# Optimization experiments

Measured on AMD Instinct MI355X. Metric: run time of the kernel, lower is better.

Reference implementation:

```python
import jax, jax.numpy as jnp
import numpy as np
import math

EPS = 1.0
DELT = 1e-05
CLIP = 1.0
N_LOCS = 1000000
EMB_DIM = 64
N_EDGES = 4000000


def setup_inputs() -> dict:
    key = jax.random.key(0)
    k1, k2, k3 = jax.random.split(key, 3)
    loc_emb = jax.random.normal(k1, (N_LOCS, EMB_DIM), dtype=jnp.float32)
    noise = jax.random.normal(k2, (N_EDGES, EMB_DIM), dtype=jnp.float32)
    edge_locs = jax.random.randint(k3, (N_EDGES,), 0, N_LOCS, dtype=jnp.int32)
    return {"loc_emb": loc_emb, "noise": noise, "edge_locs": edge_locs}


def reference(loc_emb, noise, edge_locs):
    n_locs = loc_emb.shape[0]
    # sigma = clip * sqrt(2 * ln(1.25/delta)) / eps  (Gaussian mechanism)
    sigma = CLIP * math.sqrt(2.0 * math.log(1.25 / DELT)) / EPS
    # edge_cnt[loc] = number of edges touching loc (Counter over real+fake)
    edge_cnt = jax.ops.segment_sum(
        jnp.ones_like(edge_locs, dtype=loc_emb.dtype), edge_locs,
        num_segments=n_locs)
    # per-edge scaled noise: sigma * n / edge_cnt[loc]; every referenced loc has cnt>=1
    inv_cnt = (sigma / edge_cnt[edge_locs])[:, None]  # [E, 1]
    loc_noise = jax.ops.segment_sum(noise * inv_cnt, edge_locs,
                                    num_segments=n_locs)  # [n_locs, d]
    return loc_emb + loc_noise
```

## Files before the change

kernel.cpp:

```cpp
#include <hip/hip_runtime.h>
#include <math.h>

#define EMB 64

typedef float f32x4 __attribute__((ext_vector_type(4)));


__global__ void count_rank_k(const int* __restrict__ el, int* __restrict__ cnt,
                             int* __restrict__ rank, int n) {
    int i = blockIdx.x * blockDim.x + threadIdx.x;
    if (i < n) rank[i] = atomicAdd(cnt + el[i], 1);
}

__global__ void block_sum_k(const int* __restrict__ cnt, int* __restrict__ part, int n) {
    __shared__ int s[256];
    int i = blockIdx.x * 256 + threadIdx.x;
    s[threadIdx.x] = (i < n) ? cnt[i] : 0;
    __syncthreads();
    for (int off = 128; off > 0; off >>= 1) {
        if (threadIdx.x < off) s[threadIdx.x] += s[threadIdx.x + off];
        __syncthreads();
    }
    if (threadIdx.x == 0) part[blockIdx.x] = s[0];
}

__global__ void scan_part_k(int* __restrict__ part, int nb) {
    __shared__ int s[4096];
    for (int i = threadIdx.x; i < 4096; i += 1024) s[i] = (i < nb) ? part[i] : 0;
    __syncthreads();
    for (int off = 1; off < 4096; off <<= 1) {
        int vals[4];
        #pragma unroll
        for (int j = 0; j < 4; ++j) {
            int i = threadIdx.x + j * 1024;
            vals[j] = (i >= off) ? s[i - off] : 0;
        }
        __syncthreads();
        #pragma unroll
        for (int j = 0; j < 4; ++j) {
            int i = threadIdx.x + j * 1024;
            s[i] += vals[j];
        }
        __syncthreads();
    }
    for (int i = threadIdx.x; i < nb; i += 1024) part[i] = (i == 0) ? 0 : s[i - 1];
}

__global__ void scan_block_k(const int* __restrict__ cnt, const int* __restrict__ part,
                             int* __restrict__ offs, int n) {
    __shared__ int s[256];
    int i = blockIdx.x * 256 + threadIdx.x;
    int v = (i < n) ? cnt[i] : 0;
    s[threadIdx.x] = v;
    __syncthreads();
    for (int off = 1; off < 256; off <<= 1) {
        int t = (threadIdx.x >= (unsigned)off) ? s[threadIdx.x - off] : 0;
        __syncthreads();
        s[threadIdx.x] += t;
        __syncthreads();
    }
    if (i < n) offs[i] = s[threadIdx.x] - v + part[blockIdx.x];
}

__global__ void fill_csr_k(const int* __restrict__ el, const int* __restrict__ rank,
                           const int* __restrict__ offs, int* __restrict__ csr, int n) {
    int i = blockIdx.x * blockDim.x + threadIdx.x;
    if (i < n) csr[offs[el[i]] + rank[i]] = i;
}


__device__ __forceinline__ f32x4 ld_row(const float* noise, int e, int q) {
    return *(reinterpret_cast<const f32x4*>(noise + ((long long)e << 6)) + q);
}

__global__ void gather_k(const float* __restrict__ loc_emb, const float* __restrict__ noise,
                         const int* __restrict__ cnt, const int* __restrict__ offs,
                         const int* __restrict__ csr, float* __restrict__ out,
                         float sigma, int n_locs) {
    int gid = blockIdx.x * blockDim.x + threadIdx.x;
    int loc = gid >> 4;
    if (loc >= n_locs) return;
    int q = gid & 15;
    int c = cnt[loc];
    int st = offs[loc];
    f32x4 acc = (f32x4)(0.f);
    for (int i = 0; i < c; i += 8) {
        int r = c - i;
        int b0 = st + i;
        int e[8];
        #pragma unroll
        for (int j = 0; j < 8; ++j)
            e[j] = csr[b0 + (j < r ? j : r - 1)];
        f32x4 v[8];
        #pragma unroll
        for (int j = 0; j < 8; ++j)
            v[j] = ld_row(noise, e[j], q);
        #pragma unroll
        for (int j = 0; j < 8; ++j)
            if (j < r) acc += v[j];
    }
    float s = (c > 0) ? sigma / (float)c : 0.f;
    const f32x4* bp = reinterpret_cast<const f32x4*>(loc_emb + ((long long)loc << 6)) + q;
    f32x4 b = __builtin_nontemporal_load(bp);
    f32x4 o = b + s * acc;
    f32x4* op = reinterpret_cast<f32x4*>(out + ((long long)loc << 6)) + q;
    __builtin_nontemporal_store(o, op);
}

extern "C" void kernel_launch(void* const* d_in, const int* in_sizes, int n_in,
                              void* d_out, int out_size, void* d_ws, size_t ws_size,
                              hipStream_t stream) {
    const float* loc_emb = (const float*)d_in[0];
    const float* noise   = (const float*)d_in[1];
    const int*   el      = (const int*)d_in[2];
    float* out = (float*)d_out;

    int n_locs  = in_sizes[0] / EMB;
    int n_edges = in_sizes[2];

    char* w = (char*)d_ws;
    int* cnt  = (int*)w;                 w += (size_t)n_locs * sizeof(int);
    int* offs = (int*)w;                 w += (size_t)n_locs * sizeof(int);
    int* part = (int*)w;                 w += 4096 * sizeof(int);
    int* rank = (int*)w;                 w += (size_t)n_edges * sizeof(int);
    int* csr  = (int*)w;

    int nb = (n_locs + 255) / 256;

    (void)hipMemsetAsync(cnt, 0, (size_t)n_locs * sizeof(int), stream);

    count_rank_k<<<(n_edges + 255) / 256, 256, 0, stream>>>(el, cnt, rank, n_edges);
    block_sum_k<<<nb, 256, 0, stream>>>(cnt, part, n_locs);
    scan_part_k<<<1, 1024, 0, stream>>>(part, nb);
    scan_block_k<<<nb, 256, 0, stream>>>(cnt, part, offs, n_locs);
    fill_csr_k<<<(n_edges + 255) / 256, 256, 0, stream>>>(el, rank, offs, csr, n_edges);

    double sigma = 1.0 * sqrt(2.0 * log(1.25 / 1e-5)) / 1.0;
    long long total = (long long)n_locs * 16;
    int blocks = (int)((total + 255) / 256);
    gather_k<<<blocks, 256, 0, stream>>>(loc_emb, noise, cnt, offs, csr, out,
                                         (float)sigma, n_locs);
}
```

Measured before the change: 541.9 us.

## Vectorize edge kernels, pack offset/count metadata, gather two locations per thread

The count/rank and CSR-fill kernels now handle four edges per thread with 128-bit loads and stores. Offsets and counts are packed into one int2 metadata array, so the gather reads both in a single vector load. The gather kernel now handles two locations per 16-lane group, which gives each thread more independent noise-row loads in flight, and it uses nontemporal loads for noise. The cost is extra wasted loads when the two locations have unequal counts. Edge indices are also clamped for safety, and the n4 tail logic assumes el and rank can be read as full 16-byte vectors.

New measurement: 605.7 us. 11.8% more time.

```diff
diff --git a/kernel.cpp b/kernel.cpp
--- a/kernel.cpp
+++ b/kernel.cpp
@@ -4,12 +4,21 @@
 #define EMB 64
 
 typedef float f32x4 __attribute__((ext_vector_type(4)));
+typedef int   i32x4 __attribute__((ext_vector_type(4)));
 
 
 __global__ void count_rank_k(const int* __restrict__ el, int* __restrict__ cnt,
-                             int* __restrict__ rank, int n) {
+                             int* __restrict__ rank, int n4, int n) {
     int i = blockIdx.x * blockDim.x + threadIdx.x;
-    if (i < n) rank[i] = atomicAdd(cnt + el[i], 1);
+    if (i >= n4) return;
+    int base = i * 4;
+    i32x4 e = __builtin_nontemporal_load(reinterpret_cast<const i32x4*>(el) + i);
+    i32x4 r;
+    r.x = atomicAdd(cnt + e.x, 1);
+    r.y = (base + 1 < n) ? atomicAdd(cnt + e.y, 1) : 0;
+    r.z = (base + 2 < n) ? atomicAdd(cnt + e.z, 1) : 0;
+    r.w = (base + 3 < n) ? atomicAdd(cnt + e.w, 1) : 0;
+    __builtin_nontemporal_store(r, reinterpret_cast<i32x4*>(rank) + i);
 }
 
 __global__ void block_sum_k(const int* __restrict__ cnt, int* __restrict__ part, int n) {
@@ -46,8 +55,8 @@
     for (int i = threadIdx.x; i < nb; i += 1024) part[i] = (i == 0) ? 0 : s[i - 1];
 }
 
-__global__ void scan_block_k(const int* __restrict__ cnt, const int* __restrict__ part,
-                             int* __restrict__ offs, int n) {
+__global__ void scan_meta_k(const int* __restrict__ cnt, const int* __restrict__ part,
+                            int2* __restrict__ meta, int n) {
     __shared__ int s[256];
     int i = blockIdx.x * 256 + threadIdx.x;
     int v = (i < n) ? cnt[i] : 0;
@@ -59,52 +68,83 @@
         s[threadIdx.x] += t;
         __syncthreads();
     }
-    if (i < n) offs[i] = s[threadIdx.x] - v + part[blockIdx.x];
+    if (i < n) {
+        int2 m;
+        m.x = s[threadIdx.x] - v + part[blockIdx.x];
+        m.y = v;
+        meta[i] = m;
+    }
 }
 
 __global__ void fill_csr_k(const int* __restrict__ el, const int* __restrict__ rank,
-                           const int* __restrict__ offs, int* __restrict__ csr, int n) {
+                           const int2* __restrict__ meta, int* __restrict__ csr,
+                           int n4, int n) {
     int i = blockIdx.x * blockDim.x + threadIdx.x;
-    if (i < n) csr[offs[el[i]] + rank[i]] = i;
+    if (i >= n4) return;
+    int base = i * 4;
+    i32x4 e = __builtin_nontemporal_load(reinterpret_cast<const i32x4*>(el) + i);
+    i32x4 r = __builtin_nontemporal_load(reinterpret_cast<const i32x4*>(rank) + i);
+    csr[meta[e.x].x + r.x] = base;
+    if (base + 1 < n) csr[meta[e.y].x + r.y] = base + 1;
+    if (base + 2 < n) csr[meta[e.z].x + r.z] = base + 2;
+    if (base + 3 < n) csr[meta[e.w].x + r.w] = base + 3;
 }
 
 
-__device__ __forceinline__ f32x4 ld_row(const float* noise, int e, int q) {
-    return *(reinterpret_cast<const f32x4*>(noise + ((long long)e << 6)) + q);
+__device__ __forceinline__ f32x4 ld_row_nt(const float* noise, int e, int q) {
+    const f32x4* p = reinterpret_cast<const f32x4*>(noise + ((long long)e << 6)) + q;
+    return __builtin_nontemporal_load(p);
 }
 
-__global__ void gather_k(const float* __restrict__ loc_emb, const float* __restrict__ noise,
-                         const int* __restrict__ cnt, const int* __restrict__ offs,
-                         const int* __restrict__ csr, float* __restrict__ out,
-                         float sigma, int n_locs) {
+__global__ void gather2_k(const float* __restrict__ loc_emb, const float* __restrict__ noise,
+                          const int* __restrict__ meta, const int* __restrict__ csr,
+                          float* __restrict__ out, float sigma, int n_locs, int n_edges) {
     int gid = blockIdx.x * blockDim.x + threadIdx.x;
-    int loc = gid >> 4;
-    if (loc >= n_locs) return;
+    int g = gid >> 4;
     int q = gid & 15;
-    int c = cnt[loc];
-    int st = offs[loc];
-    f32x4 acc = (f32x4)(0.f);
-    for (int i = 0; i < c; i += 8) {
-        int r = c - i;
-        int b0 = st + i;
-        int e[8];
+    int loc0 = g * 2;
+    if (loc0 >= n_locs) return;
+    i32x4 m = *(reinterpret_cast<const i32x4*>(meta) + g);
+    int st0 = m.x, c0 = m.y, st1 = m.z, c1 = m.w;
+    int cmax = c0 > c1 ? c0 : c1;
+    int l0 = c0 > 0 ? c0 - 1 : 0;
+    int l1 = c1 > 0 ? c1 - 1 : 0;
+    f32x4 a0 = (f32x4)(0.f), a1 = (f32x4)(0.f);
+    for (int i = 0; i < cmax; i += 8) {
+        int e0[8], e1[8];
         #pragma unroll
-        for (int j = 0; j < 8; ++j)
-            e[j] = csr[b0 + (j < r ? j : r - 1)];
-        f32x4 v[8];
+        for (int j = 0; j < 8; ++j) {
+            int i0 = i + j;
+            int k0 = st0 + (i0 < l0 ? i0 : l0);
+            int k1 = st1 + (i0 < l1 ? i0 : l1);
+            int t0 = csr[k0];
+            int t1 = csr[k1];
+            e0[j] = ((unsigned)t0 < (unsigned)n_edges) ? t0 : 0;
+            e1[j] = ((unsigned)t1 < (unsigned)n_edges) ? t1 : 0;
+        }
+        f32x4 v0[8], v1[8];
         #pragma unroll
-        for (int j = 0; j < 8; ++j)
-            v[j] = ld_row(noise, e[j], q);
+        for (int j = 0; j < 8; ++j) {
+            v0[j] = ld_row_nt(noise, e0[j], q);
+            v1[j] = ld_row_nt(noise, e1[j], q);
+        }
         #pragma unroll
-        for (int j = 0; j < 8; ++j)
-            if (j < r) acc += v[j];
+        for (int j = 0; j < 8; ++j) {
+            if (i + j < c0) a0 += v0[j];
+            if (i + j < c1) a1 += v1[j];
+        }
     }
-    float s = (c > 0) ? sigma / (float)c : 0.f;
-    const f32x4* bp = reinterpret_cast<const f32x4*>(loc_emb + ((long long)loc << 6)) + q;
-    f32x4 b = __builtin_nontemporal_load(bp);
-    f32x4 o = b + s * acc;
-    f32x4* op = reinterpret_cast<f32x4*>(out + ((long long)loc << 6)) + q;
-    __builtin_nontemporal_store(o, op);
+    float s0 = (c0 > 0) ? sigma / (float)c0 : 0.f;
+    float s1 = (c1 > 0) ? sigma / (float)c1 : 0.f;
+    long long base = ((long long)loc0 << 6) + (q << 2);
+    f32x4 b0 = __builtin_nontemporal_load(reinterpret_cast<const f32x4*>(loc_emb + base));
+    f32x4 o0 = b0 + s0 * a0;
+    __builtin_nontemporal_store(o0, reinterpret_cast<f32x4*>(out + base));
+    if (loc0 + 1 < n_locs) {
+        f32x4 b1 = __builtin_nontemporal_load(reinterpret_cast<const f32x4*>(loc_emb + base + EMB));
+        f32x4 o1 = b1 + s1 * a1;
+        __builtin_nontemporal_store(o1, reinterpret_cast<f32x4*>(out + base + EMB));
+    }
 }
 
 extern "C" void kernel_launch(void* const* d_in, const int* in_sizes, int n_in,
@@ -119,25 +159,27 @@
     int n_edges = in_sizes[2];
 
     char* w = (char*)d_ws;
-    int* cnt  = (int*)w;                 w += (size_t)n_locs * sizeof(int);
-    int* offs = (int*)w;                 w += (size_t)n_locs * sizeof(int);
-    int* part = (int*)w;                 w += 4096 * sizeof(int);
-    int* rank = (int*)w;                 w += (size_t)n_edges * sizeof(int);
-    int* csr  = (int*)w;
+    int*  cnt  = (int*)w;                 w += (size_t)n_locs * sizeof(int);
+    int*  part = (int*)w;                 w += 4096 * sizeof(int);
+    int2* meta = (int2*)w;                w += (size_t)n_locs * sizeof(int2);
+    int*  rank = (int*)w;                 w += (size_t)n_edges * sizeof(int);
+    int*  csr  = (int*)w;
 
     int nb = (n_locs + 255) / 256;
+    int n4 = (n_edges + 3) / 4;
 
     (void)hipMemsetAsync(cnt, 0, (size_t)n_locs * sizeof(int), stream);
 
-    count_rank_k<<<(n_edges + 255) / 256, 256, 0, stream>>>(el, cnt, rank, n_edges);
+    count_rank_k<<<(n4 + 255) / 256, 256, 0, stream>>>(el, cnt, rank, n4, n_edges);
     block_sum_k<<<nb, 256, 0, stream>>>(cnt, part, n_locs);
     scan_part_k<<<1, 1024, 0, stream>>>(part, nb);
-    scan_block_k<<<nb, 256, 0, stream>>>(cnt, part, offs, n_locs);
-    fill_csr_k<<<(n_edges + 255) / 256, 256, 0, stream>>>(el, rank, offs, csr, n_edges);
+    scan_meta_k<<<nb, 256, 0, stream>>>(cnt, part, meta, n_locs);
+    fill_csr_k<<<(n4 + 255) / 256, 256, 0, stream>>>(el, rank, meta, csr, n4, n_edges);
 
     double sigma = 1.0 * sqrt(2.0 * log(1.25 / 1e-5)) / 1.0;
-    long long total = (long long)n_locs * 16;
+    int n_groups = (n_locs + 1) / 2;
+    long long total = (long long)n_groups * 16;
     int blocks = (int)((total + 255) / 256);
-    gather_k<<<blocks, 256, 0, stream>>>(loc_emb, noise, cnt, offs, csr, out,
-                                         (float)sigma, n_locs);
+    gather2_k<<<blocks, 256, 0, stream>>>(loc_emb, noise, (const int*)meta, csr, out,
+                                          (float)sigma, n_locs, n_edges);
 }
```
